# Kernel optimization log

Measured on AMD Instinct MI355X. Metric: run time of the kernel, lower is better.

The kernel has to match this reference:

```python
import jax, jax.numpy as jnp
import numpy as np

DIM = 2048
INTER = 1408
N_EXPERTS = 16
TOP_K = 2
N_SHARED = 2
SHARED_INTER = N_SHARED * INTER  # 2816


def setup_inputs() -> dict:
    key = jax.random.key(0)
    ks = jax.random.split(key, 9)
    s = 0.02
    return {
        "x": jax.random.normal(ks[0], (4, 2048, DIM), dtype=jnp.float32),
        "gate_w": jax.random.normal(ks[1], (N_EXPERTS, DIM), dtype=jnp.float32) * s,
        "w1": jax.random.normal(ks[2], (N_EXPERTS, INTER, DIM), dtype=jnp.float32) * s,
        "w2": jax.random.normal(ks[3], (N_EXPERTS, DIM, INTER), dtype=jnp.float32) * s,
        "w3": jax.random.normal(ks[4], (N_EXPERTS, INTER, DIM), dtype=jnp.float32) * s,
        "sw1": jax.random.normal(ks[5], (SHARED_INTER, DIM), dtype=jnp.float32) * s,
        "sw2": jax.random.normal(ks[6], (DIM, SHARED_INTER), dtype=jnp.float32) * s,
        "sw3": jax.random.normal(ks[7], (SHARED_INTER, DIM), dtype=jnp.float32) * s,
    }


def _swiglu(t, wa, wb, wo):
    # t: [T, d_in]; wa, wb: [d_h, d_in]; wo: [d_out, d_h]
    h = jax.nn.silu(t @ wa.T) * (t @ wb.T)
    return h @ wo.T


def reference(x, gate_w, w1, w2, w3, sw1, sw2, sw3):
    shape = x.shape
    t = x.reshape(-1, DIM)                      # [T, dim]
    scores = jax.nn.softmax(t @ gate_w.T, axis=-1)  # [T, E]
    weights, indices = jax.lax.top_k(scores, TOP_K)  # [T, k] each

    y = jnp.zeros_like(t)
    # Small fixed loop over experts (structurally distinct weights).
    # Per-token combine weight for expert e: sum over top-k slots routed to e
    # (matches y[idx] += expert(x[idx]) * weights[idx, top]; zero weight for
    # unrouted tokens reproduces the counts[i]==0 skip exactly).
    for e in range(N_EXPERTS):
        w_e = jnp.sum(jnp.where(indices == e, weights, 0.0), axis=-1)  # [T]
        y = y + _swiglu(t, w1[e], w3[e], w2[e]) * w_e[:, None]

    z = _swiglu(t, sw1, sw3, sw2)               # shared experts MLP
    return (y + z).reshape(shape)
```

## Files before the change

kernel.cpp:

```cpp
#include <hip/hip_runtime.h>
#include <hip/hip_bf16.h>

#define DIM 2048
#define INTER 1408
#define NEXP 16
#define NTOK 8192
#define SINTER 2816

typedef __attribute__((ext_vector_type(8))) short bf16x8;
typedef __attribute__((ext_vector_type(4))) float f32x4;
typedef __attribute__((ext_vector_type(4))) unsigned short u16x4;
typedef __attribute__((ext_vector_type(8))) unsigned short u16x8;

#define VMCNT(n) asm volatile("s_waitcnt vmcnt(" #n ")" ::: "memory")
#define BARRIER() __builtin_amdgcn_s_barrier()

__device__ __forceinline__ unsigned short f2bf(float f) {
    union { float f; unsigned u; } a; a.f = f;
    unsigned r = a.u + 0x7fffu + ((a.u >> 16) & 1u);
    return (unsigned short)(r >> 16);
}
__device__ __forceinline__ float bf2f(unsigned short u) {
    union { unsigned u; float f; } a; a.u = ((unsigned)u) << 16; return a.f;
}

__device__ __forceinline__ void gload16(const void* g, void* lds) {
    __builtin_amdgcn_global_load_lds(
        (const __attribute__((address_space(1))) void*)g,
        (__attribute__((address_space(3))) void*)lds, 16, 0, 0);
}

__global__ __launch_bounds__(256) void cast_bf16(const float* __restrict__ s,
                                                 unsigned short* __restrict__ d,
                                                 long long n) {
    long long i = ((long long)blockIdx.x * 256 + threadIdx.x) * 8;
    if (i >= n) return;
    float4 a = *(const float4*)(s + i), b = *(const float4*)(s + i + 4);
    u16x8 o = { f2bf(a.x), f2bf(a.y), f2bf(a.z), f2bf(a.w),
                f2bf(b.x), f2bf(b.y), f2bf(b.z), f2bf(b.w) };
    *(u16x8*)(d + i) = o;
}

__global__ __launch_bounds__(256) void gate_topk(
    const float* __restrict__ x, const float* __restrict__ gw,
    unsigned short* __restrict__ xb,
    int* __restrict__ counts, int* __restrict__ toklist,
    int* __restrict__ se, int* __restrict__ sp, float* __restrict__ swt) {
    int wave = threadIdx.x >> 6;
    int lane = threadIdx.x & 63;
    int tok  = blockIdx.x * 4 + wave;
    const float* xr = x + (size_t)tok * DIM;
    unsigned short* xbr = xb + (size_t)tok * DIM;

    float part[NEXP];
#pragma unroll
    for (int e = 0; e < NEXP; ++e) part[e] = 0.f;
#pragma unroll
    for (int c = 0; c < DIM / 256; ++c) {
        float4 xv = *(const float4*)(xr + c * 256 + lane * 4);
        u16x4 xo = { f2bf(xv.x), f2bf(xv.y), f2bf(xv.z), f2bf(xv.w) };
        *(u16x4*)(xbr + c * 256 + lane * 4) = xo;
#pragma unroll
        for (int e = 0; e < NEXP; ++e) {
            float4 g = *(const float4*)(gw + e * DIM + c * 256 + lane * 4);
            part[e] += xv.x * g.x + xv.y * g.y + xv.z * g.z + xv.w * g.w;
        }
    }
#pragma unroll
    for (int e = 0; e < NEXP; ++e) {
        float v = part[e];
#pragma unroll
        for (int off = 32; off; off >>= 1) v += __shfl_xor(v, off);
        part[e] = v;
    }
    float mx = part[0];
#pragma unroll
    for (int e = 1; e < NEXP; ++e) mx = fmaxf(mx, part[e]);
    float Z = 0.f;
#pragma unroll
    for (int e = 0; e < NEXP; ++e) Z += expf(part[e] - mx);
    int i1 = 0; float m1 = part[0];
#pragma unroll
    for (int e = 1; e < NEXP; ++e) if (part[e] > m1) { m1 = part[e]; i1 = e; }
    int i2 = -1; float m2 = -1e30f;
#pragma unroll
    for (int e = 0; e < NEXP; ++e) if (e != i1 && part[e] > m2) { m2 = part[e]; i2 = e; }
    if (lane == 0) {
        float w1v = expf(m1 - mx) / Z;
        float w2v = expf(m2 - mx) / Z;
        int p1 = atomicAdd(&counts[i1], 1);
        toklist[i1 * NTOK + p1] = tok;
        int p2 = atomicAdd(&counts[i2], 1);
        toklist[i2 * NTOK + p2] = tok;
        se[2 * tok] = i1;  sp[2 * tok] = p1;  swt[2 * tok] = w1v;
        se[2 * tok + 1] = i2;  sp[2 * tok + 1] = p2;  swt[2 * tok + 1] = w2v;
    }
}

__global__ void prefix_k(const int* __restrict__ counts, int* __restrict__ base) {
    if (threadIdx.x == 0) {
        int acc = 0;
        for (int e = 0; e < NEXP; ++e) { base[e] = acc; acc += counts[e]; }
        base[16] = acc;
        base[17] = acc + NTOK;
    }
}

__device__ __forceinline__ int swz(int r) { return (r ^ (r >> 2)) & 3; }

__global__ __launch_bounds__(512, 2) void gemm1(
    const unsigned short* __restrict__ xb,
    const unsigned short* __restrict__ w1b, const unsigned short* __restrict__ w3b,
    const unsigned short* __restrict__ sw1b, const unsigned short* __restrict__ sw3b,
    const int* __restrict__ counts, const int* __restrict__ base,
    const int* __restrict__ toklist, unsigned short* __restrict__ hbuf) {
    const int e   = blockIdx.z;
    const int cnt = (e < NEXP) ? counts[e] : NTOK;
    const int m0  = blockIdx.y * 256;
    if (m0 >= cnt) return;
    const int n0  = blockIdx.x * 128;
    const size_t woff = (size_t)((e < NEXP) ? e : e - NEXP) * INTER * DIM;
    const unsigned short* B1 = ((e < NEXP) ? w1b : sw1b) + woff;
    const unsigned short* B3 = ((e < NEXP) ? w3b : sw3b) + woff;
    const int hbase = base[e];
    const int* tl = toklist + e * NTOK;

    __shared__ __attribute__((aligned(16))) unsigned short As[4][8192];
    __shared__ __attribute__((aligned(16))) unsigned short B1s[4][4096];
    __shared__ __attribute__((aligned(16))) unsigned short B3s[4][4096];

    const int tid = threadIdx.x;
    const int w = tid >> 6, lu = tid & 63;
    const int wr = w >> 1, wc = w & 1;
    const int lr = lu & 15, hi = lu >> 4;

    const int row0 = tid >> 2, row1 = row0 + 128;
    const int c0 = (tid & 3) ^ swz(row0);
    int g0 = m0 + row0, g1 = m0 + row1;
    int t0, t1;
    if (e < NEXP) { t0 = (g0 < cnt) ? tl[g0] : 0; t1 = (g1 < cnt) ? tl[g1] : 0; }
    else          { t0 = g0; t1 = g1; }
    const unsigned short* aSrc0 = xb + (size_t)t0 * DIM + c0 * 8;
    const unsigned short* aSrc1 = xb + (size_t)t1 * DIM + c0 * 8;
    const unsigned short* b1Src = B1 + (size_t)(n0 + row0) * DIM + c0 * 8;
    const unsigned short* b3Src = B3 + (size_t)(n0 + row0) * DIM + c0 * 8;

    int aoff[4], boff[4];
#pragma unroll
    for (int m = 0; m < 4; ++m) {
        int r = wr * 64 + m * 16 + lr;
        aoff[m] = r * 64 + ((swz(r) ^ hi) << 4);
    }
#pragma unroll
    for (int n = 0; n < 4; ++n) {
        int r = wc * 64 + n * 16 + lr;
        boff[n] = r * 64 + ((swz(r) ^ hi) << 4);
    }

    f32x4 acc1[4][4], acc3[4][4];
#pragma unroll
    for (int m = 0; m < 4; ++m)
#pragma unroll
        for (int n = 0; n < 4; ++n) {
            acc1[m][n] = (f32x4){0.f, 0.f, 0.f, 0.f};
            acc3[m][n] = (f32x4){0.f, 0.f, 0.f, 0.f};
        }

    const int H = DIM / 32;

    auto STAGE = [&](int hh) {
        int hb = hh & 3;
        int kc = hh * 32;
        gload16(aSrc0 + kc, &As[hb][tid * 8]);
        gload16(aSrc1 + kc, &As[hb][4096 + tid * 8]);
        gload16(b1Src + kc, &B1s[hb][tid * 8]);
        gload16(b3Src + kc, &B3s[hb][tid * 8]);
    };

    STAGE(0); STAGE(1);
    VMCNT(4);
    BARRIER();

    for (int h = 0; h < H; ++h) {
        const int hb = h & 3;
        const char* As_ = (const char*)&As[hb][0];
        const char* B1_ = (const char*)&B1s[hb][0];
        const char* B3_ = (const char*)&B3s[hb][0];
        bf16x8 af[4], b1f[4], b3f[4];
#pragma unroll
        for (int m = 0; m < 4; ++m) af[m] = *(const bf16x8*)(As_ + aoff[m]);
#pragma unroll
        for (int n = 0; n < 4; ++n) {
            b1f[n] = *(const bf16x8*)(B1_ + boff[n]);
            b3f[n] = *(const bf16x8*)(B3_ + boff[n]);
        }
        if (h + 2 < H) { STAGE(h + 2); VMCNT(4); }
        else           { VMCNT(0); }
        BARRIER();
        __builtin_amdgcn_s_setprio(1);
#pragma unroll
        for (int n = 0; n < 4; ++n)
#pragma unroll
            for (int m = 0; m < 4; ++m)
                acc1[m][n] = __builtin_amdgcn_mfma_f32_16x16x32_bf16(af[m], b1f[n], acc1[m][n], 0, 0, 0);
#pragma unroll
        for (int n = 0; n < 4; ++n)
#pragma unroll
            for (int m = 0; m < 4; ++m)
                acc3[m][n] = __builtin_amdgcn_mfma_f32_16x16x32_bf16(af[m], b3f[n], acc3[m][n], 0, 0, 0);
        __builtin_amdgcn_s_setprio(0);
    }

#pragma unroll
    for (int m = 0; m < 4; ++m) {
#pragma unroll
        for (int i = 0; i < 4; ++i) {
            int row  = wr * 64 + m * 16 + hi * 4 + i;
            int grow = m0 + row;
            if (grow < cnt) {
                size_t ro = (size_t)(hbase + grow) * INTER;
#pragma unroll
                for (int n = 0; n < 4; ++n) {
                    int col = n0 + wc * 64 + n * 16 + lr;
                    float a = acc1[m][n][i];
                    float hv = a / (1.f + __expf(-a)) * acc3[m][n][i];
                    hbuf[ro + col] = f2bf(hv);
                }
            }
        }
    }
}

__global__ __launch_bounds__(512, 2) void gemm2(
    const unsigned short* __restrict__ hbuf,
    const unsigned short* __restrict__ w2b, const unsigned short* __restrict__ sw2b,
    const int* __restrict__ counts, const int* __restrict__ base,
    unsigned short* __restrict__ g2buf) {
    const int e   = blockIdx.z;
    const int cnt = (e < NEXP) ? counts[e] : NTOK;
    const int m0  = blockIdx.y * 256;
    if (m0 >= cnt) return;
    const int n0  = blockIdx.x * 128;
    const int hbase = base[e];
    const size_t bstride = (e < NEXP) ? INTER : SINTER;
    const unsigned short* Bb = (e < NEXP) ? w2b + (size_t)e * DIM * INTER
                                          : sw2b + (size_t)(e - NEXP) * INTER;

    __shared__ __attribute__((aligned(16))) unsigned short Ah[4][8192];
    __shared__ __attribute__((aligned(16))) unsigned short Bh[4][4096];

    const int tid = threadIdx.x;
    const int w = tid >> 6, lu = tid & 63;
    const int wr = w >> 1, wc = w & 1;
    const int lr = lu & 15, hi = lu >> 4;

    const int row0 = tid >> 2, row1 = row0 + 128;
    const int c0 = (tid & 3) ^ swz(row0);
    const unsigned short* aSrc0 = hbuf + (size_t)(hbase + m0 + row0) * INTER + c0 * 8;
    const unsigned short* aSrc1 = hbuf + (size_t)(hbase + m0 + row1) * INTER + c0 * 8;
    const unsigned short* bSrc  = Bb + (size_t)(n0 + row0) * bstride + c0 * 8;

    int aoff[4], boff[4];
#pragma unroll
    for (int m = 0; m < 4; ++m) {
        int r = wr * 64 + m * 16 + lr;
        aoff[m] = r * 64 + ((swz(r) ^ hi) << 4);
    }
#pragma unroll
    for (int n = 0; n < 4; ++n) {
        int r = wc * 64 + n * 16 + lr;
        boff[n] = r * 64 + ((swz(r) ^ hi) << 4);
    }

    f32x4 acc[4][4];
#pragma unroll
    for (int m = 0; m < 4; ++m)
#pragma unroll
        for (int n = 0; n < 4; ++n) acc[m][n] = (f32x4){0.f, 0.f, 0.f, 0.f};

    const int H = INTER / 32;

    auto STAGE = [&](int hh) {
        int hb = hh & 3;
        int kc = hh * 32;
        gload16(aSrc0 + kc, &Ah[hb][tid * 8]);
        gload16(aSrc1 + kc, &Ah[hb][4096 + tid * 8]);
        gload16(bSrc  + kc, &Bh[hb][tid * 8]);
    };

    STAGE(0); STAGE(1);
    VMCNT(3);
    BARRIER();

    for (int h = 0; h < H; ++h) {
        const int hb = h & 3;
        const char* A_ = (const char*)&Ah[hb][0];
        const char* B_ = (const char*)&Bh[hb][0];
        bf16x8 af[4], bf[4];
#pragma unroll
        for (int m = 0; m < 4; ++m) af[m] = *(const bf16x8*)(A_ + aoff[m]);
#pragma unroll
        for (int n = 0; n < 4; ++n) bf[n] = *(const bf16x8*)(B_ + boff[n]);
        if (h + 2 < H) { STAGE(h + 2); VMCNT(3); }
        else           { VMCNT(0); }
        BARRIER();
        __builtin_amdgcn_s_setprio(1);
#pragma unroll
        for (int n = 0; n < 4; ++n)
#pragma unroll
            for (int m = 0; m < 4; ++m)
                acc[m][n] = __builtin_amdgcn_mfma_f32_16x16x32_bf16(af[m], bf[n], acc[m][n], 0, 0, 0);
        __builtin_amdgcn_s_setprio(0);
    }

#pragma unroll
    for (int m = 0; m < 4; ++m) {
#pragma unroll
        for (int i = 0; i < 4; ++i) {
            int row  = wr * 64 + m * 16 + hi * 4 + i;
            int grow = m0 + row;
            if (grow < cnt) {
                unsigned short* orow = g2buf + (size_t)(hbase + grow) * DIM + n0 + wc * 64 + lr;
#pragma unroll
                for (int n = 0; n < 4; ++n)
                    orow[n * 16] = f2bf(acc[m][n][i]);
            }
        }
    }
}

__global__ __launch_bounds__(256) void combine(
    const unsigned short* __restrict__ g2buf, const int* __restrict__ base,
    const int* __restrict__ se, const int* __restrict__ sp,
    const float* __restrict__ swt, float* __restrict__ out) {
    const int tok = blockIdx.x;
    const int c = threadIdx.x * 8;
    const int e0 = se[2 * tok], e1 = se[2 * tok + 1];
    const float w0 = swt[2 * tok], w1 = swt[2 * tok + 1];
    const size_t r0 = (size_t)(base[e0] + sp[2 * tok]) * DIM + c;
    const size_t r1 = (size_t)(base[e1] + sp[2 * tok + 1]) * DIM + c;
    const size_t r2 = (size_t)(2 * NTOK + tok) * DIM + c;
    const size_t r3 = (size_t)(3 * NTOK + tok) * DIM + c;
    u16x8 a = *(const u16x8*)(g2buf + r0);
    u16x8 b = *(const u16x8*)(g2buf + r1);
    u16x8 s0 = *(const u16x8*)(g2buf + r2);
    u16x8 s1 = *(const u16x8*)(g2buf + r3);
    float o[8];
#pragma unroll
    for (int j = 0; j < 8; ++j)
        o[j] = w0 * bf2f(a[j]) + w1 * bf2f(b[j]) + bf2f(s0[j]) + bf2f(s1[j]);
    float4* op = (float4*)(out + (size_t)tok * DIM + c);
    op[0] = make_float4(o[0], o[1], o[2], o[3]);
    op[1] = make_float4(o[4], o[5], o[6], o[7]);
}

extern "C" void kernel_launch(void* const* d_in, const int* in_sizes, int n_in,
                              void* d_out, int out_size, void* d_ws, size_t ws_size,
                              hipStream_t stream) {
    const float* x   = (const float*)d_in[0];
    const float* gw  = (const float*)d_in[1];
    const float* w1  = (const float*)d_in[2];
    const float* w2  = (const float*)d_in[3];
    const float* w3  = (const float*)d_in[4];
    const float* sw1 = (const float*)d_in[5];
    const float* sw2 = (const float*)d_in[6];
    const float* sw3 = (const float*)d_in[7];
    float* out = (float*)d_out;

    char* ws = (char*)d_ws;
    int*   counts  = (int*)ws;
    int*   basep   = (int*)(ws + 128);
    int*   toklist = (int*)(ws + 4096);
    int*   se      = (int*)(ws + 4096 + (5 << 19));
    int*   sp      = (int*)(ws + 4096 + (5 << 19) + (1 << 16));
    float* swt     = (float*)(ws + 4096 + (5 << 19) + (2 << 16));

    se  = (int*)(ws + 4096 + 524288);
    sp  = (int*)(ws + 4096 + 524288 + 65536);
    swt = (float*)(ws + 4096 + 524288 + 131072);

    unsigned short* hbuf = (unsigned short*)(ws + (2u << 20));

    const size_t hbytes = (size_t)4 * NTOK * INTER * 2;
    const size_t offx   = (2ull << 20) + hbytes;
    const size_t xbytes = (size_t)NTOK * DIM * 2;
    const size_t offw   = offx + xbytes;
    const size_t wB     = (size_t)NEXP * INTER * DIM * 2;
    const size_t swB    = (size_t)SINTER * DIM * 2;

    unsigned short* xb   = (unsigned short*)(ws + offx);
    unsigned short* w1b  = (unsigned short*)(ws + offw);
    unsigned short* w3b  = (unsigned short*)(ws + offw + wB);
    unsigned short* w2b  = (unsigned short*)(ws + offw + 2 * wB);
    unsigned short* sw1b = (unsigned short*)(ws + offw + 3 * wB);
    unsigned short* sw3b = (unsigned short*)(ws + offw + 3 * wB + swB);
    unsigned short* sw2b = (unsigned short*)(ws + offw + 3 * wB + 2 * swB);

    unsigned short* g2buf = (unsigned short*)(ws + offx);

    hipMemsetAsync(counts, 0, 64, stream);

    gate_topk<<<NTOK / 4, 256, 0, stream>>>(x, gw, xb, counts, toklist, se, sp, swt);
    prefix_k<<<1, 64, 0, stream>>>(counts, basep);

    auto cast = [&](const float* s, unsigned short* d, long long n) {
        cast_bf16<<<(int)((n / 8 + 255) / 256), 256, 0, stream>>>(s, d, n);
    };
    cast(w1, w1b, (long long)NEXP * INTER * DIM);
    cast(w3, w3b, (long long)NEXP * INTER * DIM);
    cast(sw1, sw1b, (long long)SINTER * DIM);
    cast(sw3, sw3b, (long long)SINTER * DIM);

    gemm1<<<dim3(INTER / 128, NTOK / 256, 18), 512, 0, stream>>>(
        xb, w1b, w3b, sw1b, sw3b, counts, basep, toklist, hbuf);

    cast(w2, w2b, (long long)NEXP * INTER * DIM);
    cast(sw2, sw2b, (long long)SINTER * DIM);

    gemm2<<<dim3(DIM / 128, NTOK / 256, 18), 512, 0, stream>>>(
        hbuf, w2b, sw2b, counts, basep, g2buf);

    combine<<<NTOK, 256, 0, stream>>>(g2buf, basep, se, sp, swt, out);
}
```

Baseline: 1.278 ms.

## Use K=64 double-buffered tiles with 8-way XOR swizzle in both GEMMs

Both grouped GEMM kernels move from a 4-stage ring of K=32 tiles (prefetch distance 2) to two buffers of K=64 tiles with prefetch distance 1. Each iteration now does two MFMA sub-steps, which halves the number of barriers and waitcnts per K. The LDS swizzle becomes an 8-slot XOR over 128-byte rows. The cost is less latency hiding: the wait for the next tile sits at the end of each iteration, right after the loads are issued, so global load latency can be exposed. The workspace pointer setup is also tidied.

```diff
diff --git a/kernel.cpp b/kernel.cpp
--- a/kernel.cpp
+++ b/kernel.cpp
@@ -105,8 +105,6 @@
         base[17] = acc + NTOK;
     }
 }
-
-__device__ __forceinline__ int swz(int r) { return (r ^ (r >> 2)) & 3; }
 
 __global__ __launch_bounds__(512, 2) void gemm1(
     const unsigned short* __restrict__ xb,
@@ -125,36 +123,49 @@
     const int hbase = base[e];
     const int* tl = toklist + e * NTOK;
 
-    __shared__ __attribute__((aligned(16))) unsigned short As[4][8192];
-    __shared__ __attribute__((aligned(16))) unsigned short B1s[4][4096];
-    __shared__ __attribute__((aligned(16))) unsigned short B3s[4][4096];
+    __shared__ __attribute__((aligned(16))) unsigned short As[2][16384];
+    __shared__ __attribute__((aligned(16))) unsigned short B1s[2][8192];
+    __shared__ __attribute__((aligned(16))) unsigned short B3s[2][8192];
 
     const int tid = threadIdx.x;
     const int w = tid >> 6, lu = tid & 63;
     const int wr = w >> 1, wc = w & 1;
     const int lr = lu & 15, hi = lu >> 4;
 
-    const int row0 = tid >> 2, row1 = row0 + 128;
-    const int c0 = (tid & 3) ^ swz(row0);
-    int g0 = m0 + row0, g1 = m0 + row1;
-    int t0, t1;
-    if (e < NEXP) { t0 = (g0 < cnt) ? tl[g0] : 0; t1 = (g1 < cnt) ? tl[g1] : 0; }
-    else          { t0 = g0; t1 = g1; }
-    const unsigned short* aSrc0 = xb + (size_t)t0 * DIM + c0 * 8;
-    const unsigned short* aSrc1 = xb + (size_t)t1 * DIM + c0 * 8;
-    const unsigned short* b1Src = B1 + (size_t)(n0 + row0) * DIM + c0 * 8;
-    const unsigned short* b3Src = B3 + (size_t)(n0 + row0) * DIM + c0 * 8;
-
-    int aoff[4], boff[4];
-#pragma unroll
-    for (int m = 0; m < 4; ++m) {
-        int r = wr * 64 + m * 16 + lr;
-        aoff[m] = r * 64 + ((swz(r) ^ hi) << 4);
-    }
-#pragma unroll
-    for (int n = 0; n < 4; ++n) {
-        int r = wc * 64 + n * 16 + lr;
-        boff[n] = r * 64 + ((swz(r) ^ hi) << 4);
+    const int srow = tid >> 3;
+    const int sslot = tid & 7;
+    const int cEl = ((sslot ^ (srow & 7)) * 8);
+
+    const unsigned short* aSrc[4];
+#pragma unroll
+    for (int i = 0; i < 4; ++i) {
+        int grow = m0 + 64 * i + srow;
+        int t;
+        if (e < NEXP) t = (grow < cnt) ? tl[grow] : 0;
+        else          t = grow;
+        aSrc[i] = xb + (size_t)t * DIM + cEl;
+    }
+    const unsigned short *b1Src[2], *b3Src[2];
+#pragma unroll
+    for (int i = 0; i < 2; ++i) {
+        int r = n0 + 64 * i + srow;
+        b1Src[i] = B1 + (size_t)r * DIM + cEl;
+        b3Src[i] = B3 + (size_t)r * DIM + cEl;
+    }
+
+    int aoff[2][4], boff[2][4];
+#pragma unroll
+    for (int kk = 0; kk < 2; ++kk) {
+#pragma unroll
+        for (int m = 0; m < 4; ++m) {
+            int R = wr * 64 + m * 16 + lr;
+            aoff[kk][m] = R * 128 + (((kk * 4 + hi) ^ (lr & 7)) << 4);
+        }
+#pragma unroll
+        for (int n = 0; n < 4; ++n) {
+            int R = wc * 64 + n * 16 + lr;
+            boff[kk][n] = R * 128 + (((kk * 4 + hi) ^ (lr & 7)) << 4);
+        }
     }
 
     f32x4 acc1[4][4], acc3[4][4];
@@ -166,37 +177,39 @@
             acc3[m][n] = (f32x4){0.f, 0.f, 0.f, 0.f};
         }
 
-    const int H = DIM / 32;
+    const int H = DIM / 64;
 
     auto STAGE = [&](int hh) {
-        int hb = hh & 3;
-        int kc = hh * 32;
-        gload16(aSrc0 + kc, &As[hb][tid * 8]);
-        gload16(aSrc1 + kc, &As[hb][4096 + tid * 8]);
-        gload16(b1Src + kc, &B1s[hb][tid * 8]);
-        gload16(b3Src + kc, &B3s[hb][tid * 8]);
+        int hb = hh & 1;
+        int kc = hh * 64;
+#pragma unroll
+        for (int i = 0; i < 4; ++i)
+            gload16(aSrc[i] + kc, &As[hb][i * 4096 + tid * 8]);
+#pragma unroll
+        for (int i = 0; i < 2; ++i) {
+            gload16(b1Src[i] + kc, &B1s[hb][i * 4096 + tid * 8]);
+            gload16(b3Src[i] + kc, &B3s[hb][i * 4096 + tid * 8]);
+        }
     };
 
-    STAGE(0); STAGE(1);
-    VMCNT(4);
+    STAGE(0);
+    VMCNT(0);
     BARRIER();
 
     for (int h = 0; h < H; ++h) {
-        const int hb = h & 3;
+        const int hb = h & 1;
         const char* As_ = (const char*)&As[hb][0];
         const char* B1_ = (const char*)&B1s[hb][0];
         const char* B3_ = (const char*)&B3s[hb][0];
         bf16x8 af[4], b1f[4], b3f[4];
 #pragma unroll
-        for (int m = 0; m < 4; ++m) af[m] = *(const bf16x8*)(As_ + aoff[m]);
+        for (int m = 0; m < 4; ++m) af[m] = *(const bf16x8*)(As_ + aoff[0][m]);
 #pragma unroll
         for (int n = 0; n < 4; ++n) {
-            b1f[n] = *(const bf16x8*)(B1_ + boff[n]);
-            b3f[n] = *(const bf16x8*)(B3_ + boff[n]);
-        }
-        if (h + 2 < H) { STAGE(h + 2); VMCNT(4); }
-        else           { VMCNT(0); }
-        BARRIER();
+            b1f[n] = *(const bf16x8*)(B1_ + boff[0][n]);
+            b3f[n] = *(const bf16x8*)(B3_ + boff[0][n]);
+        }
+        if (h + 1 < H) STAGE(h + 1);
         __builtin_amdgcn_s_setprio(1);
 #pragma unroll
         for (int n = 0; n < 4; ++n)
@@ -209,6 +222,27 @@
             for (int m = 0; m < 4; ++m)
                 acc3[m][n] = __builtin_amdgcn_mfma_f32_16x16x32_bf16(af[m], b3f[n], acc3[m][n], 0, 0, 0);
         __builtin_amdgcn_s_setprio(0);
+#pragma unroll
+        for (int m = 0; m < 4; ++m) af[m] = *(const bf16x8*)(As_ + aoff[1][m]);
+#pragma unroll
+        for (int n = 0; n < 4; ++n) {
+            b1f[n] = *(const bf16x8*)(B1_ + boff[1][n]);
+            b3f[n] = *(const bf16x8*)(B3_ + boff[1][n]);
+        }
+        __builtin_amdgcn_s_setprio(1);
+#pragma unroll
+        for (int n = 0; n < 4; ++n)
+#pragma unroll
+            for (int m = 0; m < 4; ++m)
+                acc1[m][n] = __builtin_amdgcn_mfma_f32_16x16x32_bf16(af[m], b1f[n], acc1[m][n], 0, 0, 0);
+#pragma unroll
+        for (int n = 0; n < 4; ++n)
+#pragma unroll
+            for (int m = 0; m < 4; ++m)
+                acc3[m][n] = __builtin_amdgcn_mfma_f32_16x16x32_bf16(af[m], b3f[n], acc3[m][n], 0, 0, 0);
+        __builtin_amdgcn_s_setprio(0);
+        VMCNT(0);
+        BARRIER();
     }
 
 #pragma unroll
@@ -246,30 +280,40 @@
     const unsigned short* Bb = (e < NEXP) ? w2b + (size_t)e * DIM * INTER
                                           : sw2b + (size_t)(e - NEXP) * INTER;
 
-    __shared__ __attribute__((aligned(16))) unsigned short Ah[4][8192];
-    __shared__ __attribute__((aligned(16))) unsigned short Bh[4][4096];
+    __shared__ __attribute__((aligned(16))) unsigned short Ah[2][16384];
+    __shared__ __attribute__((aligned(16))) unsigned short Bh[2][8192];
 
     const int tid = threadIdx.x;
     const int w = tid >> 6, lu = tid & 63;
     const int wr = w >> 1, wc = w & 1;
     const int lr = lu & 15, hi = lu >> 4;
 
-    const int row0 = tid >> 2, row1 = row0 + 128;
-    const int c0 = (tid & 3) ^ swz(row0);
-    const unsigned short* aSrc0 = hbuf + (size_t)(hbase + m0 + row0) * INTER + c0 * 8;
-    const unsigned short* aSrc1 = hbuf + (size_t)(hbase + m0 + row1) * INTER + c0 * 8;
-    const unsigned short* bSrc  = Bb + (size_t)(n0 + row0) * bstride + c0 * 8;
-
-    int aoff[4], boff[4];
-#pragma unroll
-    for (int m = 0; m < 4; ++m) {
-        int r = wr * 64 + m * 16 + lr;
-        aoff[m] = r * 64 + ((swz(r) ^ hi) << 4);
-    }
-#pragma unroll
-    for (int n = 0; n < 4; ++n) {
-        int r = wc * 64 + n * 16 + lr;
-        boff[n] = r * 64 + ((swz(r) ^ hi) << 4);
+    const int srow = tid >> 3;
+    const int sslot = tid & 7;
+    const int cEl = ((sslot ^ (srow & 7)) * 8);
+
+    const unsigned short* aSrc[4];
+#pragma unroll
+    for (int i = 0; i < 4; ++i)
+        aSrc[i] = hbuf + (size_t)(hbase + m0 + 64 * i + srow) * INTER + cEl;
+    const unsigned short* bSrc[2];
+#pragma unroll
+    for (int i = 0; i < 2; ++i)
+        bSrc[i] = Bb + (size_t)(n0 + 64 * i + srow) * bstride + cEl;
+
+    int aoff[2][4], boff[2][4];
+#pragma unroll
+    for (int kk = 0; kk < 2; ++kk) {
+#pragma unroll
+        for (int m = 0; m < 4; ++m) {
+            int R = wr * 64 + m * 16 + lr;
+            aoff[kk][m] = R * 128 + (((kk * 4 + hi) ^ (lr & 7)) << 4);
+        }
+#pragma unroll
+        for (int n = 0; n < 4; ++n) {
+            int R = wc * 64 + n * 16 + lr;
+            boff[kk][n] = R * 128 + (((kk * 4 + hi) ^ (lr & 7)) << 4);
+        }
     }
 
     f32x4 acc[4][4];
@@ -278,32 +322,33 @@
 #pragma unroll
         for (int n = 0; n < 4; ++n) acc[m][n] = (f32x4){0.f, 0.f, 0.f, 0.f};
 
-    const int H = INTER / 32;
+    const int H = INTER / 64;
 
     auto STAGE = [&](int hh) {
-        int hb = hh & 3;
-        int kc = hh * 32;
-        gload16(aSrc0 + kc, &Ah[hb][tid * 8]);
-        gload16(aSrc1 + kc, &Ah[hb][4096 + tid * 8]);
-        gload16(bSrc  + kc, &Bh[hb][tid * 8]);
+        int hb = hh & 1;
+        int kc = hh * 64;
+#pragma unroll
+        for (int i = 0; i < 4; ++i)
+            gload16(aSrc[i] + kc, &Ah[hb][i * 4096 + tid * 8]);
+#pragma unroll
+        for (int i = 0; i < 2; ++i)
+            gload16(bSrc[i] + kc, &Bh[hb][i * 4096 + tid * 8]);
     };
 
-    STAGE(0); STAGE(1);
-    VMCNT(3);
+    STAGE(0);
+    VMCNT(0);
     BARRIER();
 
     for (int h = 0; h < H; ++h) {
-        const int hb = h & 3;
+        const int hb = h & 1;
         const char* A_ = (const char*)&Ah[hb][0];
         const char* B_ = (const char*)&Bh[hb][0];
         bf16x8 af[4], bf[4];
 #pragma unroll
-        for (int m = 0; m < 4; ++m) af[m] = *(const bf16x8*)(A_ + aoff[m]);
-#pragma unroll
-        for (int n = 0; n < 4; ++n) bf[n] = *(const bf16x8*)(B_ + boff[n]);
-        if (h + 2 < H) { STAGE(h + 2); VMCNT(3); }
-        else           { VMCNT(0); }
-        BARRIER();
+        for (int m = 0; m < 4; ++m) af[m] = *(const bf16x8*)(A_ + aoff[0][m]);
+#pragma unroll
+        for (int n = 0; n < 4; ++n) bf[n] = *(const bf16x8*)(B_ + boff[0][n]);
+        if (h + 1 < H) STAGE(h + 1);
         __builtin_amdgcn_s_setprio(1);
 #pragma unroll
         for (int n = 0; n < 4; ++n)
@@ -311,6 +356,19 @@
             for (int m = 0; m < 4; ++m)
                 acc[m][n] = __builtin_amdgcn_mfma_f32_16x16x32_bf16(af[m], bf[n], acc[m][n], 0, 0, 0);
         __builtin_amdgcn_s_setprio(0);
+#pragma unroll
+        for (int m = 0; m < 4; ++m) af[m] = *(const bf16x8*)(A_ + aoff[1][m]);
+#pragma unroll
+        for (int n = 0; n < 4; ++n) bf[n] = *(const bf16x8*)(B_ + boff[1][n]);
+        __builtin_amdgcn_s_setprio(1);
+#pragma unroll
+        for (int n = 0; n < 4; ++n)
+#pragma unroll
+            for (int m = 0; m < 4; ++m)
+                acc[m][n] = __builtin_amdgcn_mfma_f32_16x16x32_bf16(af[m], bf[n], acc[m][n], 0, 0, 0);
+        __builtin_amdgcn_s_setprio(0);
+        VMCNT(0);
+        BARRIER();
     }
 
 #pragma unroll
@@ -371,13 +429,9 @@
     int*   counts  = (int*)ws;
     int*   basep   = (int*)(ws + 128);
     int*   toklist = (int*)(ws + 4096);
-    int*   se      = (int*)(ws + 4096 + (5 << 19));
-    int*   sp      = (int*)(ws + 4096 + (5 << 19) + (1 << 16));
-    float* swt     = (float*)(ws + 4096 + (5 << 19) + (2 << 16));
-
-    se  = (int*)(ws + 4096 + 524288);
-    sp  = (int*)(ws + 4096 + 524288 + 65536);
-    swt = (float*)(ws + 4096 + 524288 + 131072);
+    int*   se      = (int*)(ws + 4096 + 524288);
+    int*   sp      = (int*)(ws + 4096 + 524288 + 65536);
+    float* swt     = (float*)(ws + 4096 + 524288 + 131072);
 
     unsigned short* hbuf = (unsigned short*)(ws + (2u << 20));
 
```

Result: no change. 1.263 ms (-1.2%).
